# Kernel tuning notes

Measured on AMD Instinct MI355X. Metric: run time of the kernel, lower is better.

## Reference

```python
import jax, jax.numpy as jnp
import numpy as np

B, D, CTX, H = 8192, 64, 256, 512  # batch, latent dim (made.nin), context dim, MADE hidden


def _masks(D, H):
    """Standard MADE natural-ordering masks (Germain et al. 2015)."""
    m0 = np.arange(1, D + 1)                 # input degrees 1..D
    mh = (np.arange(H) % (D - 1)) + 1        # hidden degrees 1..D-1
    M1 = (mh[:, None] >= m0[None, :]).astype(np.float32)   # (H, D)
    M2 = (mh[:, None] >= mh[None, :]).astype(np.float32)   # (H, H)
    mo = np.concatenate([m0, m0])            # outputs = [means; pre_scales]
    Mo = (mo[:, None] > mh[None, :]).astype(np.float32)    # (2D, H)
    return jnp.asarray(M1), jnp.asarray(M2), jnp.asarray(Mo)


def setup_inputs() -> dict:
    key = jax.random.key(0)
    ks = jax.random.split(key, 7)
    s = 0.05
    return {
        "context": jax.random.normal(ks[0], (B, CTX), jnp.float32),
        "eps": jax.random.normal(ks[1], (B, D), jnp.float32),  # reparameterization noise
        "W1": jax.random.normal(ks[2], (H, D), jnp.float32) * s,
        "b1": jnp.zeros((H,), jnp.float32),
        "Wc": jax.random.normal(ks[3], (H, CTX), jnp.float32) * s,
        "W2": jax.random.normal(ks[4], (H, H), jnp.float32) * s,
        "b2": jnp.zeros((H,), jnp.float32),
        "Wo": jax.random.normal(ks[5], (2 * D, H), jnp.float32) * s,
        "bo": jnp.zeros((2 * D,), jnp.float32),
    }


def reference(context, eps, W1, b1, Wc, W2, b2, Wo, bo):
    """AutoRegressiveDistribution.rsample (gaussian): D sequential MADE forwards,
    each extracting column i of (mu, softplus(pre_scale)) and sampling z_i."""
    M1, M2, Mo = _masks(D, H)
    W1m, W2m, Wom = (W1 * M1).T, (W2 * M2).T, (Wo * Mo).T
    ctx_h = context @ Wc.T  # context projection is constant across steps

    def step(z, i):
        h = jax.nn.relu(z @ W1m + ctx_h + b1)   # (B, H)
        h = jax.nn.relu(h @ W2m + b2)           # (B, H)
        out = h @ Wom + bo                      # (B, 2D): [means | pre_scales]
        mu_i = out[:, i]
        scale_i = jax.nn.softplus(out[:, D + i])
        z_i = mu_i + scale_i * eps[:, i]        # Normal(mu, scale).rsample()
        z = z.at[:, i].set(z_i)
        return z, (mu_i, scale_i)

    z0 = jnp.zeros((context.shape[0], D), context.dtype)
    z, (mus, scales) = jax.lax.scan(step, z0, jnp.arange(D))
    # state = (z_sample, mu_inferred, scale_inferred), each (B, D)
    return z, mus.T, scales.T
```

## Files before the change

kernel.cpp:

```cpp
#include <hip/hip_runtime.h>
#include <math.h>


typedef float f2 __attribute__((ext_vector_type(2)));

#define Bn 8192
#define Dn 64
#define CTXn 256
#define Hn 512
#define On 128
#define Rn 8

#define WQ_SZ  (64 * 512 * 12)
#define WOQ_SZ (64 * 64 * 20)
#define WCP_SZ (CTXn * Hn)

#define BARRIER() do {                                      \
    asm volatile("s_waitcnt lgkmcnt(0)" ::: "memory");      \
    __builtin_amdgcn_s_barrier();                           \
    asm volatile("" ::: "memory");                          \
  } while (0)

__device__ __forceinline__ int perm_of(int p, int* degout) {
  int k, t;
  if (p < 72) { k = p / 9 + 1; t = p - (k - 1) * 9; }
  else        { int pp = p - 72; k = pp / 8 + 9; t = pp - (k - 9) * 8; }
  *degout = k;
  return (k - 1) + 63 * t;
}
__device__ __forceinline__ int inv_perm(int h) {
  int i = h % 63;
  int t = h / 63;
  int base = (i < 9) ? 9 * i : 72 + 8 * (i - 8);
  return base + t;
}

#define R0e 262144
#define R1e (R0e + 32768)
#define R2e (R1e + 65536)
#define R3e (R2e + 131072)
#define R4e (R3e + 35840)
#define R5e (R4e + 1024)
__global__ void prep_kernel(const float* __restrict__ W1, const float* __restrict__ Wc,
                            const float* __restrict__ W2, const float* __restrict__ Wo,
                            const float* __restrict__ b1, const float* __restrict__ b2,
                            float* __restrict__ Wq, float* __restrict__ Woq,
                            float* __restrict__ WcpT, float* __restrict__ b1p,
                            float* __restrict__ b2p) {
  int idx = blockIdx.x * 256 + threadIdx.x;
  if (idx < R0e) {
    int hq = idx >> 9, hp = idx & 511;
    int i = hp % 63, e = hp / 63;
    Wq[i * 6144 + inv_perm(hq) * 12 + e] = W2[idx];
  } else if (idx < R1e) {
    int jj = idx - R0e;
    int hq = jj >> 6, i = jj & 63;
    Wq[i * 6144 + inv_perm(hq) * 12 + 9] = W1[jj];
  } else if (idx < R2e) {
    int jj = idx - R1e;
    int o = jj >> 9, hp = jj & 511;
    int i = hp % 63, p = hp / 63;
    int j = o & 63, half = o >> 6;
    Woq[i * 1280 + j * 20 + half * 10 + p] = Wo[jj];
  } else if (idx < R3e) {
    int jj = idx - R2e;
    int hq = jj >> 8, cc = jj & 255;
    int p = inv_perm(hq);
    int slot = (p < 256) ? (2 * p) : (2 * (p - 256) + 1);
    WcpT[cc * 512 + slot] = Wc[jj];
  } else if (idx < R4e) {
    int z = idx - R3e;
    if (z < 28672) {
      int i = 8 + (z >> 9), q = z & 511;
      Wq[i * 6144 + q * 12 + 8] = 0.f;
    } else {
      int z2 = z - 28672;
      int i = 8 + (z2 >> 7), r = z2 & 127;
      int j = r & 63, half = r >> 6;
      Woq[i * 1280 + j * 20 + half * 10 + 8] = 0.f;
    }
  } else if (idx < R5e) {
    int z = idx - R4e;
    if (z < 512) {
      int dq; int hq = perm_of(z, &dq);
      b1p[z] = b1[hq];
    } else {
      int q = z - 512;
      int dq; int hq = perm_of(q, &dq);
      b2p[q] = b2[hq];
    }
  }
}

__global__ __launch_bounds__(256, 4)
void made_pk_kernel(
    const float* __restrict__ context, const float* __restrict__ WcpT,
    const float* __restrict__ b1p,
    const float* __restrict__ Wq, const float* __restrict__ Woq,
    const float* __restrict__ b2p, const float* __restrict__ bo,
    const float* __restrict__ eps, float* __restrict__ out) {
  __shared__ __align__(16) float ctxR[8][264];
  __shared__ __align__(16) float zcur[8];
  __shared__ __align__(16) float h1g[9][8];
  __shared__ __align__(16) float h2g[9][8];

  int t = threadIdx.x;
  int b0 = blockIdx.x * Rn;
  int rp = t >> 6, l = t & 63;
  int q0 = t, q1 = t + 256;

  int g0 = ((q0 < 72) ? q0 / 9 + 1 : (q0 - 72) / 8 + 9) - 1;
  int g1 = ((q1 - 72) / 8 + 9) - 1;
  int qm = t | 63;
  int gm0s = __builtin_amdgcn_readfirstlane(
      ((qm < 72) ? qm / 9 + 1 : (qm - 72) / 8 + 9) - 1);
  int gm1s = __builtin_amdgcn_readfirstlane(((qm + 256 - 72) / 8 + 9) - 1);

  #pragma unroll
  for (int r = 0; r < 8; ++r)
    ctxR[r][t] = context[(b0 + r) * CTXn + t];
  BARRIER();

  f2 accu[8];
  {
    f2 bias = (f2){b1p[q0], b1p[q1]};
    #pragma unroll
    for (int r = 0; r < 8; ++r) accu[r] = bias;
  }
  {
    const float* wc = WcpT + 2 * t;
    #pragma clang loop unroll(disable)
    for (int c4 = 0; c4 < CTXn / 4; ++c4) {
      float4 xr4[8];
      #pragma unroll
      for (int r = 0; r < 8; ++r)
        xr4[r] = *(const float4*)&ctxR[r][4 * c4];
      #pragma unroll
      for (int k = 0; k < 4; ++k) {
        f2 wv = *(const f2*)wc;
        wc += Hn;
        #pragma unroll
        for (int r = 0; r < 8; ++r) {
          float xk = (k == 0) ? xr4[r].x : (k == 1) ? xr4[r].y
                   : (k == 2) ? xr4[r].z : xr4[r].w;
          accu[r] += (f2){xk, xk} * wv;
        }
      }
    }
  }

  f2 a10[4], a11[4], a20[4], a21[4];
  #pragma unroll
  for (int r2 = 0; r2 < 4; ++r2) {
    a10[r2] = (f2){accu[2 * r2].x, accu[2 * r2 + 1].x};
    a11[r2] = (f2){accu[2 * r2].y, accu[2 * r2 + 1].y};
  }
  {
    float bb0 = b2p[q0], bb1 = b2p[q1];
    #pragma unroll
    for (int r2 = 0; r2 < 4; ++r2) {
      a20[r2] = (f2){bb0, bb0};
      a21[r2] = (f2){bb1, bb1};
    }
  }
  f2 ocA = (f2){bo[l], bo[l]};
  f2 ocB = (f2){bo[l + 64], bo[l + 64]};
  f2 ez2 = (f2){eps[(b0 + 2 * rp) * Dn + l], eps[(b0 + 2 * rp + 1) * Dn + l]};
  f2 zs = (f2){0.f, 0.f}, mus = zs, scs = zs;

  const float* wq0p = Wq + (size_t)q0 * 12;
  const float* wq1p = Wq + (size_t)q1 * 12;
  const float* wopp = Woq + (size_t)l * 20;

  #pragma clang loop unroll(disable)
  for (int i = 0; i < Dn; ++i) {
    if (l == i) {
      f2 pre = ocB;
      float sx = fmaxf(pre.x, 0.f) + __logf(1.f + __expf(-fabsf(pre.x)));
      float sy = fmaxf(pre.y, 0.f) + __logf(1.f + __expf(-fabsf(pre.y)));
      f2 sc = (f2){sx, sy};
      f2 z = ocA + sc * ez2;
      *(f2*)&zcur[2 * rp] = z;
      zs = z; mus = ocA; scs = sc;
    }
    BARRIER();

    int sb = (i < 8) ? 9 * i : 8 * i + 8;
    bool liveB = (i <= gm1s);
    bool liveA = (i <= gm0s);
    float4 A1c0, A1c1, A1c2, A0c0, A0c1, A0c2;
    if (liveB) {
      const float4* a4 = (const float4*)wq1p;
      A1c0 = a4[0]; A1c1 = a4[1]; A1c2 = a4[2];
      if (liveA) {
        const float4* b4 = (const float4*)wq0p;
        A0c0 = b4[0]; A0c1 = b4[1]; A0c2 = b4[2];
      }
      float4 za = *(const float4*)&zcur[0];
      float4 zb = *(const float4*)&zcur[4];
      f2 zc0 = (f2){za.x, za.y}, zc1 = (f2){za.z, za.w};
      f2 zc2 = (f2){zb.x, zb.y}, zc3 = (f2){zb.z, zb.w};
      {
        f2 wv = (f2){A1c2.y, A1c2.y};
        a11[0] += wv * zc0; a11[1] += wv * zc1;
        a11[2] += wv * zc2; a11[3] += wv * zc3;
        if (g1 == i) {
          int pp = q1 - sb;
          float4 h0 = {fmaxf(a11[0].x, 0.f), fmaxf(a11[0].y, 0.f),
                       fmaxf(a11[1].x, 0.f), fmaxf(a11[1].y, 0.f)};
          float4 h1_ = {fmaxf(a11[2].x, 0.f), fmaxf(a11[2].y, 0.f),
                        fmaxf(a11[3].x, 0.f), fmaxf(a11[3].y, 0.f)};
          *(float4*)&h1g[pp][0] = h0; *(float4*)&h1g[pp][4] = h1_;
        }
      }
      if (liveA) {
        f2 wv = (f2){A0c2.y, A0c2.y};
        a10[0] += wv * zc0; a10[1] += wv * zc1;
        a10[2] += wv * zc2; a10[3] += wv * zc3;
        if (g0 == i) {
          int pp = q0 - sb;
          float4 h0 = {fmaxf(a10[0].x, 0.f), fmaxf(a10[0].y, 0.f),
                       fmaxf(a10[1].x, 0.f), fmaxf(a10[1].y, 0.f)};
          float4 h1_ = {fmaxf(a10[2].x, 0.f), fmaxf(a10[2].y, 0.f),
                        fmaxf(a10[3].x, 0.f), fmaxf(a10[3].y, 0.f)};
          *(float4*)&h1g[pp][0] = h0; *(float4*)&h1g[pp][4] = h1_;
        }
      }
    }
    BARRIER();

    const float4* w4 = (const float4*)wopp;
    float4 B0 = w4[0], B1 = w4[1], B2 = w4[2], B3 = w4[3], B4 = w4[4];

    if (liveB) {
      float wA1[9] = {A1c0.x, A1c0.y, A1c0.z, A1c0.w,
                      A1c1.x, A1c1.y, A1c1.z, A1c1.w, A1c2.x};
      if (liveA) {
        float wA0[9] = {A0c0.x, A0c0.y, A0c0.z, A0c0.w,
                        A0c1.x, A0c1.y, A0c1.z, A0c1.w, A0c2.x};
        #pragma unroll
        for (int p = 0; p < 9; ++p) {
          float4 ha = *(const float4*)&h1g[p][0];
          float4 hb = *(const float4*)&h1g[p][4];
          f2 h0 = (f2){ha.x, ha.y}, h1_ = (f2){ha.z, ha.w};
          f2 h2_ = (f2){hb.x, hb.y}, h3 = (f2){hb.z, hb.w};
          f2 wv1 = (f2){wA1[p], wA1[p]};
          f2 wv0 = (f2){wA0[p], wA0[p]};
          a21[0] += wv1 * h0; a21[1] += wv1 * h1_;
          a21[2] += wv1 * h2_; a21[3] += wv1 * h3;
          a20[0] += wv0 * h0; a20[1] += wv0 * h1_;
          a20[2] += wv0 * h2_; a20[3] += wv0 * h3;
        }
      } else {
        #pragma unroll
        for (int p = 0; p < 9; ++p) {
          float4 ha = *(const float4*)&h1g[p][0];
          float4 hb = *(const float4*)&h1g[p][4];
          f2 h0 = (f2){ha.x, ha.y}, h1_ = (f2){ha.z, ha.w};
          f2 h2_ = (f2){hb.x, hb.y}, h3 = (f2){hb.z, hb.w};
          f2 wv1 = (f2){wA1[p], wA1[p]};
          a21[0] += wv1 * h0; a21[1] += wv1 * h1_;
          a21[2] += wv1 * h2_; a21[3] += wv1 * h3;
        }
      }
      if (g1 == i) {
        int pp = q1 - sb;
        float4 h0 = {fmaxf(a21[0].x, 0.f), fmaxf(a21[0].y, 0.f),
                     fmaxf(a21[1].x, 0.f), fmaxf(a21[1].y, 0.f)};
        float4 h1_ = {fmaxf(a21[2].x, 0.f), fmaxf(a21[2].y, 0.f),
                      fmaxf(a21[3].x, 0.f), fmaxf(a21[3].y, 0.f)};
        *(float4*)&h2g[pp][0] = h0; *(float4*)&h2g[pp][4] = h1_;
      }
      if (liveA && g0 == i) {
        int pp = q0 - sb;
        float4 h0 = {fmaxf(a20[0].x, 0.f), fmaxf(a20[0].y, 0.f),
                     fmaxf(a20[1].x, 0.f), fmaxf(a20[1].y, 0.f)};
        float4 h1_ = {fmaxf(a20[2].x, 0.f), fmaxf(a20[2].y, 0.f),
                      fmaxf(a20[3].x, 0.f), fmaxf(a20[3].y, 0.f)};
        *(float4*)&h2g[pp][0] = h0; *(float4*)&h2g[pp][4] = h1_;
      }
    }
    BARRIER();

    {
      float wBa[9] = {B0.x, B0.y, B0.z, B0.w, B1.x, B1.y, B1.z, B1.w, B2.x};
      float wBb[9] = {B2.z, B2.w, B3.x, B3.y, B3.z, B3.w, B4.x, B4.y, B4.z};
      #pragma unroll
      for (int p = 0; p < 9; ++p) {
        f2 h = *(const f2*)&h2g[p][2 * rp];
        ocA += (f2){wBa[p], wBa[p]} * h;
        ocB += (f2){wBb[p], wBb[p]} * h;
      }
    }
    wq0p += 6144; wq1p += 6144; wopp += 1280;
  }

  out[(b0 + 2 * rp) * Dn + l] = zs.x;
  out[(b0 + 2 * rp + 1) * Dn + l] = zs.y;
  out[Bn * Dn + (b0 + 2 * rp) * Dn + l] = mus.x;
  out[Bn * Dn + (b0 + 2 * rp + 1) * Dn + l] = mus.y;
  out[2 * Bn * Dn + (b0 + 2 * rp) * Dn + l] = scs.x;
  out[2 * Bn * Dn + (b0 + 2 * rp + 1) * Dn + l] = scs.y;
}

extern "C" void kernel_launch(void* const* d_in, const int* in_sizes, int n_in,
                              void* d_out, int out_size, void* d_ws, size_t ws_size,
                              hipStream_t stream) {
  const float* context = (const float*)d_in[0];
  const float* eps     = (const float*)d_in[1];
  const float* W1      = (const float*)d_in[2];
  const float* b1      = (const float*)d_in[3];
  const float* Wc      = (const float*)d_in[4];
  const float* W2      = (const float*)d_in[5];
  const float* b2      = (const float*)d_in[6];
  const float* Wo      = (const float*)d_in[7];
  const float* bo      = (const float*)d_in[8];
  float* out = (float*)d_out;

  float* ws   = (float*)d_ws;
  float* Wq   = ws;
  float* Woq  = Wq + WQ_SZ;
  float* WcpT = Woq + WOQ_SZ;
  float* b1p  = WcpT + WCP_SZ;
  float* b2p  = b1p + 512;

  prep_kernel<<<(R5e + 255) / 256, 256, 0, stream>>>(
      W1, Wc, W2, Wo, b1, b2, Wq, Woq, WcpT, b1p, b2p);
  made_pk_kernel<<<Bn / Rn, 256, 0, stream>>>(context, WcpT, b1p, Wq, Woq,
                                              b2p, bo, eps, out);
}
```

Measured before the change: 235.9 us.

## Use 512 threads per block with one hidden unit per thread

The block grows from 256 to 512 threads, so each thread owns a single hidden unit instead of two, and each output-stage thread handles one batch row instead of two. The context projection now reads a transposed shared context tile, and h2 is stored transposed for vectorized reads. The aim is more parallelism and less per-thread serial work in the 64-step sequential loop, at the cost of more threads waiting at barriers and higher register/LDS pressure under launch_bounds(512,8).

```diff
diff --git a/kernel.cpp b/kernel.cpp
--- a/kernel.cpp
+++ b/kernel.cpp
@@ -8,7 +8,6 @@
 #define Dn 64
 #define CTXn 256
 #define Hn 512
-#define On 128
 #define Rn 8
 
 #define WQ_SZ  (64 * 512 * 12)
@@ -65,9 +64,7 @@
   } else if (idx < R3e) {
     int jj = idx - R2e;
     int hq = jj >> 8, cc = jj & 255;
-    int p = inv_perm(hq);
-    int slot = (p < 256) ? (2 * p) : (2 * (p - 256) + 1);
-    WcpT[cc * 512 + slot] = Wc[jj];
+    WcpT[cc * 512 + inv_perm(hq)] = Wc[jj];
   } else if (idx < R4e) {
     int z = idx - R3e;
     if (z < 28672) {
@@ -92,215 +89,155 @@
   }
 }
 
-__global__ __launch_bounds__(256, 4)
+__global__ __launch_bounds__(512, 8)
 void made_pk_kernel(
     const float* __restrict__ context, const float* __restrict__ WcpT,
     const float* __restrict__ b1p,
     const float* __restrict__ Wq, const float* __restrict__ Woq,
     const float* __restrict__ b2p, const float* __restrict__ bo,
     const float* __restrict__ eps, float* __restrict__ out) {
-  __shared__ __align__(16) float ctxR[8][264];
+  __shared__ __align__(16) float ctxT[CTXn][8];
   __shared__ __align__(16) float zcur[8];
   __shared__ __align__(16) float h1g[9][8];
-  __shared__ __align__(16) float h2g[9][8];
+  __shared__ __align__(16) float h2g[8][12];
 
   int t = threadIdx.x;
   int b0 = blockIdx.x * Rn;
   int rp = t >> 6, l = t & 63;
-  int q0 = t, q1 = t + 256;
-
-  int g0 = ((q0 < 72) ? q0 / 9 + 1 : (q0 - 72) / 8 + 9) - 1;
-  int g1 = ((q1 - 72) / 8 + 9) - 1;
-  int qm = t | 63;
-  int gm0s = __builtin_amdgcn_readfirstlane(
+  int q = t;
+
+  int g = ((q < 72) ? q / 9 + 1 : (q - 72) / 8 + 9) - 1;
+  int qm = q | 63;
+  int gms = __builtin_amdgcn_readfirstlane(
       ((qm < 72) ? qm / 9 + 1 : (qm - 72) / 8 + 9) - 1);
-  int gm1s = __builtin_amdgcn_readfirstlane(((qm + 256 - 72) / 8 + 9) - 1);
 
   #pragma unroll
-  for (int r = 0; r < 8; ++r)
-    ctxR[r][t] = context[(b0 + r) * CTXn + t];
+  for (int j = 0; j < 4; ++j) {
+    int idx = t + 512 * j;
+    int r = idx >> 8, cc = idx & 255;
+    ctxT[cc][r] = context[(b0 + r) * CTXn + cc];
+  }
   BARRIER();
 
-  f2 accu[8];
+  f2 a1[4];
   {
-    f2 bias = (f2){b1p[q0], b1p[q1]};
+    float bias = b1p[q];
     #pragma unroll
-    for (int r = 0; r < 8; ++r) accu[r] = bias;
+    for (int r2 = 0; r2 < 4; ++r2) a1[r2] = (f2){bias, bias};
   }
   {
-    const float* wc = WcpT + 2 * t;
-    #pragma clang loop unroll(disable)
-    for (int c4 = 0; c4 < CTXn / 4; ++c4) {
-      float4 xr4[8];
-      #pragma unroll
-      for (int r = 0; r < 8; ++r)
-        xr4[r] = *(const float4*)&ctxR[r][4 * c4];
-      #pragma unroll
-      for (int k = 0; k < 4; ++k) {
-        f2 wv = *(const f2*)wc;
-        wc += Hn;
-        #pragma unroll
-        for (int r = 0; r < 8; ++r) {
-          float xk = (k == 0) ? xr4[r].x : (k == 1) ? xr4[r].y
-                   : (k == 2) ? xr4[r].z : xr4[r].w;
-          accu[r] += (f2){xk, xk} * wv;
-        }
-      }
-    }
-  }
-
-  f2 a10[4], a11[4], a20[4], a21[4];
-  #pragma unroll
-  for (int r2 = 0; r2 < 4; ++r2) {
-    a10[r2] = (f2){accu[2 * r2].x, accu[2 * r2 + 1].x};
-    a11[r2] = (f2){accu[2 * r2].y, accu[2 * r2 + 1].y};
-  }
+    const float* wc = WcpT + q;
+    #pragma clang loop unroll_count(4)
+    for (int cc = 0; cc < CTXn; ++cc) {
+      float w = wc[cc * Hn];
+      float4 xa = *(const float4*)&ctxT[cc][0];
+      float4 xb = *(const float4*)&ctxT[cc][4];
+      f2 wv = (f2){w, w};
+      a1[0] += wv * (f2){xa.x, xa.y};
+      a1[1] += wv * (f2){xa.z, xa.w};
+      a1[2] += wv * (f2){xb.x, xb.y};
+      a1[3] += wv * (f2){xb.z, xb.w};
+    }
+  }
+
+  f2 a2[4];
   {
-    float bb0 = b2p[q0], bb1 = b2p[q1];
+    float bb = b2p[q];
     #pragma unroll
-    for (int r2 = 0; r2 < 4; ++r2) {
-      a20[r2] = (f2){bb0, bb0};
-      a21[r2] = (f2){bb1, bb1};
-    }
-  }
-  f2 ocA = (f2){bo[l], bo[l]};
-  f2 ocB = (f2){bo[l + 64], bo[l + 64]};
-  f2 ez2 = (f2){eps[(b0 + 2 * rp) * Dn + l], eps[(b0 + 2 * rp + 1) * Dn + l]};
-  f2 zs = (f2){0.f, 0.f}, mus = zs, scs = zs;
-
-  const float* wq0p = Wq + (size_t)q0 * 12;
-  const float* wq1p = Wq + (size_t)q1 * 12;
-  const float* wopp = Woq + (size_t)l * 20;
+    for (int r2 = 0; r2 < 4; ++r2) a2[r2] = (f2){bb, bb};
+  }
+
+  float ocA = bo[l], ocB = bo[l + 64];
+  float ez = eps[(b0 + rp) * Dn + l];
+  float zs = 0.f, mus = 0.f, scs = 0.f;
+
+  const float* wqp = Wq + (size_t)q * 12;
+  const float* wop = Woq + (size_t)l * 20;
 
   #pragma clang loop unroll(disable)
   for (int i = 0; i < Dn; ++i) {
     if (l == i) {
-      f2 pre = ocB;
-      float sx = fmaxf(pre.x, 0.f) + __logf(1.f + __expf(-fabsf(pre.x)));
-      float sy = fmaxf(pre.y, 0.f) + __logf(1.f + __expf(-fabsf(pre.y)));
-      f2 sc = (f2){sx, sy};
-      f2 z = ocA + sc * ez2;
-      *(f2*)&zcur[2 * rp] = z;
+      float pre = ocB;
+      float sc = fmaxf(pre, 0.f) + __logf(1.f + __expf(-fabsf(pre)));
+      float z = ocA + sc * ez;
+      zcur[rp] = z;
       zs = z; mus = ocA; scs = sc;
     }
+    bool live = (i <= gms);
+    float4 c2;
+    if (live) c2 = *(const float4*)(wqp + 8);
     BARRIER();
 
     int sb = (i < 8) ? 9 * i : 8 * i + 8;
-    bool liveB = (i <= gm1s);
-    bool liveA = (i <= gm0s);
-    float4 A1c0, A1c1, A1c2, A0c0, A0c1, A0c2;
-    if (liveB) {
-      const float4* a4 = (const float4*)wq1p;
-      A1c0 = a4[0]; A1c1 = a4[1]; A1c2 = a4[2];
-      if (liveA) {
-        const float4* b4 = (const float4*)wq0p;
-        A0c0 = b4[0]; A0c1 = b4[1]; A0c2 = b4[2];
-      }
+    float4 c0, c1;
+    if (live) {
+      c0 = *(const float4*)wqp;
+      c1 = *(const float4*)(wqp + 4);
       float4 za = *(const float4*)&zcur[0];
       float4 zb = *(const float4*)&zcur[4];
-      f2 zc0 = (f2){za.x, za.y}, zc1 = (f2){za.z, za.w};
-      f2 zc2 = (f2){zb.x, zb.y}, zc3 = (f2){zb.z, zb.w};
-      {
-        f2 wv = (f2){A1c2.y, A1c2.y};
-        a11[0] += wv * zc0; a11[1] += wv * zc1;
-        a11[2] += wv * zc2; a11[3] += wv * zc3;
-        if (g1 == i) {
-          int pp = q1 - sb;
-          float4 h0 = {fmaxf(a11[0].x, 0.f), fmaxf(a11[0].y, 0.f),
-                       fmaxf(a11[1].x, 0.f), fmaxf(a11[1].y, 0.f)};
-          float4 h1_ = {fmaxf(a11[2].x, 0.f), fmaxf(a11[2].y, 0.f),
-                        fmaxf(a11[3].x, 0.f), fmaxf(a11[3].y, 0.f)};
-          *(float4*)&h1g[pp][0] = h0; *(float4*)&h1g[pp][4] = h1_;
-        }
-      }
-      if (liveA) {
-        f2 wv = (f2){A0c2.y, A0c2.y};
-        a10[0] += wv * zc0; a10[1] += wv * zc1;
-        a10[2] += wv * zc2; a10[3] += wv * zc3;
-        if (g0 == i) {
-          int pp = q0 - sb;
-          float4 h0 = {fmaxf(a10[0].x, 0.f), fmaxf(a10[0].y, 0.f),
-                       fmaxf(a10[1].x, 0.f), fmaxf(a10[1].y, 0.f)};
-          float4 h1_ = {fmaxf(a10[2].x, 0.f), fmaxf(a10[2].y, 0.f),
-                        fmaxf(a10[3].x, 0.f), fmaxf(a10[3].y, 0.f)};
-          *(float4*)&h1g[pp][0] = h0; *(float4*)&h1g[pp][4] = h1_;
-        }
+      f2 wv = (f2){c2.y, c2.y};
+      a1[0] += wv * (f2){za.x, za.y};
+      a1[1] += wv * (f2){za.z, za.w};
+      a1[2] += wv * (f2){zb.x, zb.y};
+      a1[3] += wv * (f2){zb.z, zb.w};
+      if (g == i) {
+        int pp = q - sb;
+        float4 h0 = {fmaxf(a1[0].x, 0.f), fmaxf(a1[0].y, 0.f),
+                     fmaxf(a1[1].x, 0.f), fmaxf(a1[1].y, 0.f)};
+        float4 h1_ = {fmaxf(a1[2].x, 0.f), fmaxf(a1[2].y, 0.f),
+                      fmaxf(a1[3].x, 0.f), fmaxf(a1[3].y, 0.f)};
+        *(float4*)&h1g[pp][0] = h0; *(float4*)&h1g[pp][4] = h1_;
       }
     }
     BARRIER();
 
-    const float4* w4 = (const float4*)wopp;
-    float4 B0 = w4[0], B1 = w4[1], B2 = w4[2], B3 = w4[3], B4 = w4[4];
-
-    if (liveB) {
-      float wA1[9] = {A1c0.x, A1c0.y, A1c0.z, A1c0.w,
-                      A1c1.x, A1c1.y, A1c1.z, A1c1.w, A1c2.x};
-      if (liveA) {
-        float wA0[9] = {A0c0.x, A0c0.y, A0c0.z, A0c0.w,
-                        A0c1.x, A0c1.y, A0c1.z, A0c1.w, A0c2.x};
-        #pragma unroll
-        for (int p = 0; p < 9; ++p) {
-          float4 ha = *(const float4*)&h1g[p][0];
-          float4 hb = *(const float4*)&h1g[p][4];
-          f2 h0 = (f2){ha.x, ha.y}, h1_ = (f2){ha.z, ha.w};
-          f2 h2_ = (f2){hb.x, hb.y}, h3 = (f2){hb.z, hb.w};
-          f2 wv1 = (f2){wA1[p], wA1[p]};
-          f2 wv0 = (f2){wA0[p], wA0[p]};
-          a21[0] += wv1 * h0; a21[1] += wv1 * h1_;
-          a21[2] += wv1 * h2_; a21[3] += wv1 * h3;
-          a20[0] += wv0 * h0; a20[1] += wv0 * h1_;
-          a20[2] += wv0 * h2_; a20[3] += wv0 * h3;
-        }
-      } else {
-        #pragma unroll
-        for (int p = 0; p < 9; ++p) {
-          float4 ha = *(const float4*)&h1g[p][0];
-          float4 hb = *(const float4*)&h1g[p][4];
-          f2 h0 = (f2){ha.x, ha.y}, h1_ = (f2){ha.z, ha.w};
-          f2 h2_ = (f2){hb.x, hb.y}, h3 = (f2){hb.z, hb.w};
-          f2 wv1 = (f2){wA1[p], wA1[p]};
-          a21[0] += wv1 * h0; a21[1] += wv1 * h1_;
-          a21[2] += wv1 * h2_; a21[3] += wv1 * h3;
-        }
-      }
-      if (g1 == i) {
-        int pp = q1 - sb;
-        float4 h0 = {fmaxf(a21[0].x, 0.f), fmaxf(a21[0].y, 0.f),
-                     fmaxf(a21[1].x, 0.f), fmaxf(a21[1].y, 0.f)};
-        float4 h1_ = {fmaxf(a21[2].x, 0.f), fmaxf(a21[2].y, 0.f),
-                      fmaxf(a21[3].x, 0.f), fmaxf(a21[3].y, 0.f)};
-        *(float4*)&h2g[pp][0] = h0; *(float4*)&h2g[pp][4] = h1_;
-      }
-      if (liveA && g0 == i) {
-        int pp = q0 - sb;
-        float4 h0 = {fmaxf(a20[0].x, 0.f), fmaxf(a20[0].y, 0.f),
-                     fmaxf(a20[1].x, 0.f), fmaxf(a20[1].y, 0.f)};
-        float4 h1_ = {fmaxf(a20[2].x, 0.f), fmaxf(a20[2].y, 0.f),
-                      fmaxf(a20[3].x, 0.f), fmaxf(a20[3].y, 0.f)};
-        *(float4*)&h2g[pp][0] = h0; *(float4*)&h2g[pp][4] = h1_;
-      }
-    }
-    BARRIER();
-
-    {
-      float wBa[9] = {B0.x, B0.y, B0.z, B0.w, B1.x, B1.y, B1.z, B1.w, B2.x};
-      float wBb[9] = {B2.z, B2.w, B3.x, B3.y, B3.z, B3.w, B4.x, B4.y, B4.z};
+    if (live) {
+      float wA[9] = {c0.x, c0.y, c0.z, c0.w, c1.x, c1.y, c1.z, c1.w, c2.x};
       #pragma unroll
       for (int p = 0; p < 9; ++p) {
-        f2 h = *(const f2*)&h2g[p][2 * rp];
-        ocA += (f2){wBa[p], wBa[p]} * h;
-        ocB += (f2){wBb[p], wBb[p]} * h;
-      }
-    }
-    wq0p += 6144; wq1p += 6144; wopp += 1280;
-  }
-
-  out[(b0 + 2 * rp) * Dn + l] = zs.x;
-  out[(b0 + 2 * rp + 1) * Dn + l] = zs.y;
-  out[Bn * Dn + (b0 + 2 * rp) * Dn + l] = mus.x;
-  out[Bn * Dn + (b0 + 2 * rp + 1) * Dn + l] = mus.y;
-  out[2 * Bn * Dn + (b0 + 2 * rp) * Dn + l] = scs.x;
-  out[2 * Bn * Dn + (b0 + 2 * rp + 1) * Dn + l] = scs.y;
+        float4 ha = *(const float4*)&h1g[p][0];
+        float4 hb = *(const float4*)&h1g[p][4];
+        f2 wv = (f2){wA[p], wA[p]};
+        a2[0] += wv * (f2){ha.x, ha.y};
+        a2[1] += wv * (f2){ha.z, ha.w};
+        a2[2] += wv * (f2){hb.x, hb.y};
+        a2[3] += wv * (f2){hb.z, hb.w};
+      }
+      if (g == i) {
+        int pp = q - sb;
+        h2g[0][pp] = fmaxf(a2[0].x, 0.f);
+        h2g[1][pp] = fmaxf(a2[0].y, 0.f);
+        h2g[2][pp] = fmaxf(a2[1].x, 0.f);
+        h2g[3][pp] = fmaxf(a2[1].y, 0.f);
+        h2g[4][pp] = fmaxf(a2[2].x, 0.f);
+        h2g[5][pp] = fmaxf(a2[2].y, 0.f);
+        h2g[6][pp] = fmaxf(a2[3].x, 0.f);
+        h2g[7][pp] = fmaxf(a2[3].y, 0.f);
+      }
+    }
+    BARRIER();
+
+    {
+      const float4* w4 = (const float4*)wop;
+      float4 B0 = w4[0], B1 = w4[1], B2_ = w4[2], B3 = w4[3], B4 = w4[4];
+      float4 hA = *(const float4*)&h2g[rp][0];
+      float4 hB = *(const float4*)&h2g[rp][4];
+      float h8 = h2g[rp][8];
+      float wBa[9] = {B0.x, B0.y, B0.z, B0.w, B1.x, B1.y, B1.z, B1.w, B2_.x};
+      float wBb[9] = {B2_.z, B2_.w, B3.x, B3.y, B3.z, B3.w, B4.x, B4.y, B4.z};
+      float hv[9] = {hA.x, hA.y, hA.z, hA.w, hB.x, hB.y, hB.z, hB.w, h8};
+      #pragma unroll
+      for (int p = 0; p < 9; ++p) {
+        ocA = fmaf(wBa[p], hv[p], ocA);
+        ocB = fmaf(wBb[p], hv[p], ocB);
+      }
+    }
+    wqp += 6144; wop += 1280;
+  }
+
+  out[(b0 + rp) * Dn + l] = zs;
+  out[Bn * Dn + (b0 + rp) * Dn + l] = mus;
+  out[2 * Bn * Dn + (b0 + rp) * Dn + l] = scs;
 }
 
 extern "C" void kernel_launch(void* const* d_in, const int* in_sizes, int n_in,
@@ -326,6 +263,6 @@
 
   prep_kernel<<<(R5e + 255) / 256, 256, 0, stream>>>(
       W1, Wc, W2, Wo, b1, b2, Wq, Woq, WcpT, b1p, b2p);
-  made_pk_kernel<<<Bn / Rn, 256, 0, stream>>>(context, WcpT, b1p, Wq, Woq,
+  made_pk_kernel<<<Bn / Rn, 512, 0, stream>>>(context, WcpT, b1p, Wq, Woq,
                                               b2p, bo, eps, out);
 }
```

After: 358.1 us. 1.52x slower.
